# Kernel optimization log

Measured on AMD Instinct MI355X. Metric: run time of the kernel, lower is better.

## Reference

```python
import jax, jax.numpy as jnp
import numpy as np

DIM = 1024
NUM_HEADS = 16
HEAD_DIM = DIM // NUM_HEADS
SCALE = 1.0 / np.sqrt(HEAD_DIM)
B, S = 2, 2048


def setup_inputs() -> dict:
    key = jax.random.key(0)
    ks = jax.random.split(key, 10)
    std = 1.0 / np.sqrt(DIM)
    return {
        "x": jax.random.normal(ks[0], (B, S, DIM), dtype=jnp.float32),
        "Wq": jax.random.normal(ks[1], (DIM, DIM), dtype=jnp.float32) * std,
        "bq": jnp.zeros((DIM,), dtype=jnp.float32),
        "Wk": jax.random.normal(ks[2], (DIM, DIM), dtype=jnp.float32) * std,
        "bk": jnp.zeros((DIM,), dtype=jnp.float32),
        "Wv": jax.random.normal(ks[3], (DIM, DIM), dtype=jnp.float32) * std,
        "bv": jnp.zeros((DIM,), dtype=jnp.float32),
        "Wo": jax.random.normal(ks[4], (DIM, DIM), dtype=jnp.float32) * std,
        "bo": jnp.zeros((DIM,), dtype=jnp.float32),
        "mobius_weight": jax.random.normal(ks[5], (1,), dtype=jnp.float32) * 0.01,
    }


def _split_heads(t):
    b, s, _ = t.shape
    return t.reshape(b, s, NUM_HEADS, HEAD_DIM).transpose(0, 2, 1, 3)  # bhsd


def reference(x, Wq, bq, Wk, bk, Wv, bv, Wo, bo, mobius_weight):
    q = _split_heads(x @ Wq.T + bq)
    k = _split_heads(x @ Wk.T + bk)
    v = _split_heads(x @ Wv.T + bv)

    # similarity: plain QK^T
    similarity = jnp.einsum('bhqd,bhkd->bhqk', q, k)
    # mobius cross-term: q_omega . k_pi + q_pi . k_omega
    h = HEAD_DIM // 2
    q_om, q_pi = q[..., :h], q[..., h:]
    k_om, k_pi = k[..., :h], k[..., h:]
    mobius = jnp.einsum('bhqd,bhkd->bhqk', q_om, k_pi) + \
             jnp.einsum('bhqd,bhkd->bhqk', q_pi, k_om)

    incidence = (similarity + mobius_weight[0] * mobius) * SCALE
    attn = jax.nn.softmax(incidence, axis=-1)
    out = jnp.einsum('bhqk,bhkd->bhqd', attn, v)
    out = out.transpose(0, 2, 1, 3).reshape(x.shape[0], x.shape[1], DIM)
    return out @ Wo.T + bo
```

## Files before the change

### kernel.cpp

```cpp
#include <hip/hip_runtime.h>


typedef __attribute__((ext_vector_type(8))) short short8;
typedef __attribute__((ext_vector_type(4))) short s16x4;
typedef __attribute__((ext_vector_type(4))) float f32x4;
typedef __attribute__((ext_vector_type(16))) float f32x16;
typedef __attribute__((ext_vector_type(8))) __bf16 bf16x8;
typedef __attribute__((ext_vector_type(4))) unsigned uint4v;

__device__ __forceinline__ float exp2fa(float x) {
  return __builtin_amdgcn_exp2f(x);
}
__device__ __forceinline__ short f2bf(float f) {
  unsigned u = __builtin_bit_cast(unsigned, f);
  u = u + 0x7fffu + ((u >> 16) & 1u);
  return (short)(u >> 16);
}
__device__ __forceinline__ f32x4 mfma16(bf16x8 a, bf16x8 b, f32x4 c) {
  return __builtin_amdgcn_mfma_f32_16x16x32_bf16(a, b, c, 0, 0, 0);
}
__device__ __forceinline__ f32x16 mfma32(bf16x8 a, bf16x8 b, f32x16 c) {
  return __builtin_amdgcn_mfma_f32_32x32x16_bf16(a, b, c, 0, 0, 0);
}
__device__ __forceinline__ void gload_lds16(const void* g, void* l) {
  __builtin_amdgcn_global_load_lds(
      (const __attribute__((address_space(1))) unsigned int*)g,
      (__attribute__((address_space(3))) unsigned int*)l, 16, 0, 0);
}
__device__ __forceinline__ unsigned pkbf(float a, float b) {
  unsigned r;
  asm("v_cvt_pk_bf16_f32 %0, %1, %2" : "=v"(r) : "v"(a), "v"(b));
  return r;
}
__device__ __forceinline__ void plswap(unsigned& a, unsigned& b) {
  asm volatile("v_permlane32_swap_b32 %0, %1" : "+v"(a), "+v"(b));
}
__device__ __forceinline__ bf16x8 pack8(float x0, float x1, float x2, float x3,
                                        float x4, float x5, float x6, float x7) {
  unsigned a0 = pkbf(x0, x1), a1 = pkbf(x2, x3);
  unsigned a2 = pkbf(x4, x5), a3 = pkbf(x6, x7);
  plswap(a0, a2);
  plswap(a1, a3);
  uint4v u = {a0, a1, a2, a3};
  return __builtin_bit_cast(bf16x8, u);
}

__global__ void cast_all_kernel(const float* x, const float* w0, const float* w1,
                                const float* w2, const float* w3, short* xo,
                                short* o0, short* o1, short* o2, short* o3) {
  const float* in; short* out;
  const int r = blockIdx.y;
  size_t off;
  if (r < 4) { in = x; out = xo; off = (size_t)r * 131072; }
  else {
    switch (r) {
      case 4: in = w0; out = o0; break;
      case 5: in = w1; out = o1; break;
      case 6: in = w2; out = o2; break;
      default: in = w3; out = o3; break;
    }
    off = 0;
  }
  const size_t i = off + blockIdx.x * 256 + threadIdx.x;
  const float4* p = (const float4*)in;
  float4 a = p[2 * i], b = p[2 * i + 1];
  short8 o;
  o[0] = f2bf(a.x); o[1] = f2bf(a.y); o[2] = f2bf(a.z); o[3] = f2bf(a.w);
  o[4] = f2bf(b.x); o[5] = f2bf(b.y); o[6] = f2bf(b.z); o[7] = f2bf(b.w);
  ((short8*)out)[i] = o;
}

constexpr int GK = 1024, GN = 1024;
constexpr float QSCALE = 0.125f * 1.44269504088896340736f;

template <int EP>
__device__ __forceinline__ void gemm_body(char* lds, const short* __restrict__ A,
                                          const short* __restrict__ W,
                                          const float* __restrict__ bias,
                                          void* __restrict__ C,
                                          const float* __restrict__ mwp) {
  const int tid = threadIdx.x;
  const int l = tid & 63, w = tid >> 6;
  const int wr = w >> 1, wc = w & 1;
  const int m0 = blockIdx.y * 128, n0 = blockIdx.x * 128;

  f32x4 acc[4][4] = {};

  const int rg = l >> 3, c8 = l & 7;
  for (int kb = 0; kb < GK / 64; ++kb) {
    const int k0 = kb * 64;
#pragma unroll
    for (int i = 0; i < 4; ++i) {
      const int ra = i * 32 + w * 8 + rg;
      gload_lds16(A + (size_t)(m0 + ra) * GK + k0 + ((c8 ^ (ra & 7)) * 8),
                  lds + (i * 32 + w * 8) * 128);
      gload_lds16(W + (size_t)(n0 + ra) * GK + k0 + ((c8 ^ (ra & 7)) * 8),
                  lds + 16384 + (i * 32 + w * 8) * 128);
    }
    __syncthreads();
#pragma unroll
    for (int ks = 0; ks < 2; ++ks) {
      bf16x8 af[4], bfr[4];
      const int chunk = ks * 4 + (l >> 4);
#pragma unroll
      for (int mf = 0; mf < 4; ++mf) {
        const int mt = wr * 64 + mf * 16 + (l & 15);
        af[mf] = *(const bf16x8*)(lds + mt * 128 + ((chunk ^ (mt & 7)) * 16));
      }
#pragma unroll
      for (int nf = 0; nf < 4; ++nf) {
        const int nt = wc * 64 + nf * 16 + (l & 15);
        bfr[nf] = *(const bf16x8*)(lds + 16384 + nt * 128 + ((chunk ^ (nt & 7)) * 16));
      }
#pragma unroll
      for (int mf = 0; mf < 4; ++mf)
#pragma unroll
        for (int nf = 0; nf < 4; ++nf)
          acc[mf][nf] = mfma16(af[mf], bfr[nf], acc[mf][nf]);
    }
    __syncthreads();
  }

  const float mwv = (EP == 1) ? mwp[0] : 0.f;
#pragma unroll
  for (int mf = 0; mf < 4; ++mf)
#pragma unroll
    for (int nf = 0; nf < 4; ++nf) {
      const int n = n0 + wc * 64 + nf * 16 + (l & 15);
      const int mb = m0 + wr * 64 + mf * 16 + (l >> 4) * 4;
      if (EP == 2) {
        s16x4 v;
#pragma unroll
        for (int r = 0; r < 4; ++r) v[r] = f2bf(acc[mf][nf][r] + bias[n]);
        const int b = mb >> 11, s0 = mb & 2047;
        *(s16x4*)((short*)C + ((size_t)(b * 1024 + n)) * 2048 + s0) = v;
      } else {
        const float bv = bias[n];
#pragma unroll
        for (int r = 0; r < 4; ++r) {
          const int m = mb + r;
          float v = acc[mf][nf][r] + bv;
          if (EP == 0) v *= QSCALE;
          if (EP == 1) v += mwv * (acc[mf][nf ^ 2][r] + bias[n ^ 32]);
          if (EP == 3)
            ((float*)C)[(size_t)m * GN + n] = v;
          else
            ((short*)C)[(size_t)m * GN + n] = f2bf(v);
        }
      }
    }
}

__global__ __launch_bounds__(256) void gemm_qkv_kernel(
    const short* __restrict__ A, const short* Wq, const short* Wk, const short* Wv,
    const float* bq, const float* bk, const float* bv, short* q, short* kt,
    short* vt, const float* mw) {
  __shared__ __align__(16) char lds[32768];
  if (blockIdx.z == 0) gemm_body<0>(lds, A, Wq, bq, q, nullptr);
  else if (blockIdx.z == 1) gemm_body<1>(lds, A, Wk, bk, kt, mw);
  else gemm_body<2>(lds, A, Wv, bv, vt, nullptr);
}

__global__ __launch_bounds__(256) void gemm_out_kernel(const short* __restrict__ A,
                                                       const short* __restrict__ W,
                                                       const float* __restrict__ bias,
                                                       float* __restrict__ C) {
  __shared__ __align__(16) char lds[32768];
  gemm_body<3>(lds, A, W, bias, C, nullptr);
}

__global__ __launch_bounds__(512, 4) void attn_kernel(const short* __restrict__ Q,
                                                      const short* __restrict__ K,
                                                      const short* __restrict__ VT,
                                                      short* __restrict__ O) {
  constexpr int S = 2048;
  constexpr float FM = 16.0f;
  __shared__ __align__(16) char lds[4][16384];
  const int tid = threadIdx.x;
  const int l = tid & 63, w = tid >> 6;
  const int grp = w >> 2, w4 = w & 3;
  const int lo = l & 31, hi = l >> 5;
  const int bh = blockIdx.y, b = bh >> 4, h = bh & 15;
  const int q0 = blockIdx.x * 128 + w4 * 32;
  const size_t base = (size_t)b * S * 1024 + h * 64;
  const size_t vtrow0 = (size_t)(b * 1024 + h * 64);

  bf16x8 qf[4];
  {
    const short* qp = Q + base + (size_t)(q0 + lo) * 1024 + hi * 8;
#pragma unroll
    for (int ds = 0; ds < 4; ++ds) qf[ds] = *(const bf16x8*)(qp + ds * 16);
  }

  f32x16 o0 = {}, o1 = {};
  float lrow = 0.f;

  const int srow = tid >> 3, sc8 = tid & 7;
  auto STAGE = [&](int pr) {
#pragma unroll
    for (int g2 = 0; g2 < 2; ++g2) {
      const int t = 2 * pr + g2;
      char* Kd = lds[t & 3];
      char* Vd = lds[t & 3] + 8192;
      const int k0 = t * 64;
      gload_lds16(K + base + (size_t)(k0 + srow) * 1024 + ((sc8 ^ (srow & 7)) * 8),
                  Kd + w * 1024);
      gload_lds16(VT + (vtrow0 + srow) * 2048 + k0 + ((sc8 ^ (srow & 7)) * 8),
                  Vd + w * 1024);
    }
  };

  auto TILE = [&](const char* Kb, const char* Vb) {
    f32x16 st0, st1;
#pragma unroll
    for (int r = 0; r < 16; ++r) { st0[r] = -FM; st1[r] = -FM; }
    __builtin_amdgcn_s_setprio(1);
#pragma unroll
    for (int ds = 0; ds < 4; ++ds) {
      const int c = ds * 2 + hi;
      bf16x8 kf0 = *(const bf16x8*)(Kb + lo * 128 + ((c ^ (lo & 7)) * 16));
      bf16x8 kf1 = *(const bf16x8*)(Kb + (32 + lo) * 128 + ((c ^ (lo & 7)) * 16));
      st0 = mfma32(kf0, qf[ds], st0);
      st1 = mfma32(kf1, qf[ds], st1);
    }
    __builtin_amdgcn_s_setprio(0);

#pragma unroll
    for (int r = 0; r < 16; ++r) st0[r] = exp2fa(st0[r]);
#pragma unroll
    for (int r = 0; r < 16; ++r) st1[r] = exp2fa(st1[r]);
    float ts[8];
#pragma unroll
    for (int r = 0; r < 8; ++r)
      ts[r] = (st0[r] + st0[r + 8]) + (st1[r] + st1[r + 8]);
#pragma unroll
    for (int d = 4; d >= 1; d >>= 1)
#pragma unroll
      for (int r = 0; r < 4; ++r)
        if (r < d) ts[r] += ts[r + d];
    lrow += ts[0] + __shfl_xor(ts[0], 32);

    bf16x8 pf[4];
    pf[0] = pack8(st0[0], st0[1], st0[2], st0[3], st0[4], st0[5], st0[6], st0[7]);
    pf[1] = pack8(st0[8], st0[9], st0[10], st0[11], st0[12], st0[13], st0[14], st0[15]);
    pf[2] = pack8(st1[0], st1[1], st1[2], st1[3], st1[4], st1[5], st1[6], st1[7]);
    pf[3] = pack8(st1[8], st1[9], st1[10], st1[11], st1[12], st1[13], st1[14], st1[15]);

    __builtin_amdgcn_s_setprio(1);
#pragma unroll
    for (int kv = 0; kv < 4; ++kv) {
      const int c = kv * 2 + hi;
      bf16x8 vf0 = *(const bf16x8*)(Vb + lo * 128 + ((c ^ (lo & 7)) * 16));
      bf16x8 vf1 = *(const bf16x8*)(Vb + (32 + lo) * 128 + ((c ^ (lo & 7)) * 16));
      o0 = mfma32(vf0, pf[kv], o0);
      o1 = mfma32(vf1, pf[kv], o1);
    }
    __builtin_amdgcn_s_setprio(0);
  };

  STAGE(0);
  for (int p = 0; p < S / 128; ++p) {
    if (p < S / 128 - 1) {
      STAGE(p + 1);
      asm volatile("s_waitcnt vmcnt(4)" ::: "memory");
    } else {
      asm volatile("s_waitcnt vmcnt(0)" ::: "memory");
    }
    __builtin_amdgcn_s_barrier();
    const char* buf = lds[(2 * p + grp) & 3];
    TILE(buf, buf + 8192);
    asm volatile("" ::: "memory");
    __builtin_amdgcn_s_barrier();
  }

  __syncthreads();
  float* mbuf = (float*)&lds[0][0];
  float* lbuf = (float*)&lds[2][0];
  if (grp == 1) {
#pragma unroll
    for (int g = 0; g < 4; ++g) {
      const int c0 = (2 * g + hi) ^ (lo & 15);
      const int c1 = (8 + 2 * g + hi) ^ (lo & 15);
      f32x4 v0, v1;
#pragma unroll
      for (int r = 0; r < 4; ++r) { v0[r] = o0[g * 4 + r]; v1[r] = o1[g * 4 + r]; }
      *(f32x4*)(mbuf + (w4 * 32 + lo) * 64 + c0 * 4) = v0;
      *(f32x4*)(mbuf + (w4 * 32 + lo) * 64 + c1 * 4) = v1;
    }
    if (hi == 0) lbuf[w4 * 32 + lo] = lrow;
  }
  __syncthreads();
  if (grp == 0) {
#pragma unroll
    for (int g = 0; g < 4; ++g) {
      const int c0 = (2 * g + hi) ^ (lo & 15);
      const int c1 = (8 + 2 * g + hi) ^ (lo & 15);
      f32x4 v0 = *(const f32x4*)(mbuf + (w4 * 32 + lo) * 64 + c0 * 4);
      f32x4 v1 = *(const f32x4*)(mbuf + (w4 * 32 + lo) * 64 + c1 * 4);
#pragma unroll
      for (int r = 0; r < 4; ++r) { o0[g * 4 + r] += v0[r]; o1[g * 4 + r] += v1[r]; }
    }
    const float inv = 1.0f / (lrow + lbuf[w4 * 32 + lo]);
    short* Op = O + base + (size_t)(q0 + lo) * 1024;
#pragma unroll
    for (int g = 0; g < 4; ++g) {
      s16x4 v0, v1;
#pragma unroll
      for (int r = 0; r < 4; ++r) {
        v0[r] = f2bf(o0[g * 4 + r] * inv);
        v1[r] = f2bf(o1[g * 4 + r] * inv);
      }
      *(s16x4*)(Op + 8 * g + 4 * hi) = v0;
      *(s16x4*)(Op + 32 + 8 * g + 4 * hi) = v1;
    }
  }
}

extern "C" void kernel_launch(void* const* d_in, const int* in_sizes, int n_in,
                              void* d_out, int out_size, void* d_ws, size_t ws_size,
                              hipStream_t stream) {
  const float* x  = (const float*)d_in[0];
  const float* Wq = (const float*)d_in[1];
  const float* bq = (const float*)d_in[2];
  const float* Wk = (const float*)d_in[3];
  const float* bk = (const float*)d_in[4];
  const float* Wv = (const float*)d_in[5];
  const float* bv = (const float*)d_in[6];
  const float* Wo = (const float*)d_in[7];
  const float* bo = (const float*)d_in[8];
  const float* mw = (const float*)d_in[9];
  float* out = (float*)d_out;
  char* ws = (char*)d_ws;
  const size_t MB = (size_t)1 << 20;

  short* xb  = (short*)(ws + 0 * MB);
  short* wqb = (short*)(ws + 8 * MB);
  short* wkb = (short*)(ws + 10 * MB);
  short* wvb = (short*)(ws + 12 * MB);
  short* wob = (short*)(ws + 14 * MB);
  short* qb  = (short*)(ws + 16 * MB);
  short* ktb = (short*)(ws + 24 * MB);
  short* vtb = (short*)(ws + 32 * MB);
  short* ob  = (short*)(ws + 40 * MB);

  cast_all_kernel<<<dim3(512, 8), 256, 0, stream>>>(x, Wq, Wk, Wv, Wo, xb, wqb,
                                                    wkb, wvb, wob);
  gemm_qkv_kernel<<<dim3(8, 32, 3), 256, 0, stream>>>(xb, wqb, wkb, wvb, bq, bk, bv,
                                                      qb, ktb, vtb, mw);
  attn_kernel<<<dim3(16, 32), 512, 0, stream>>>(qb, ktb, vtb, ob);
  gemm_out_kernel<<<dim3(8, 32), 256, 0, stream>>>(ob, wob, bo, out);
}
```

Baseline: 131.9 us.

## Store K/V in MFMA-fragment order and load directly to registers, dropping LDS staging

The QKV GEMM epilogue now writes K and V in a pre-swizzled, fragment-ordered layout per head, so each attention lane can read its MFMA operands with contiguous 16-byte global loads. The attention kernel drops the LDS staging, barriers and waitcnt pipeline, instead prefetching the next K/V tile into registers during compute. Blocks shrink to 256 threads covering 64 queries, with a remapped 1D grid for L2 locality across heads. The kernel also removes the -16 softmax offset by initialising scores to zero. This trades LDS reuse across waves for more redundant global/L2 traffic and higher register pressure.

```diff
diff --git a/kernel.cpp b/kernel.cpp
--- a/kernel.cpp
+++ b/kernel.cpp
@@ -128,12 +128,26 @@
     for (int nf = 0; nf < 4; ++nf) {
       const int n = n0 + wc * 64 + nf * 16 + (l & 15);
       const int mb = m0 + wr * 64 + mf * 16 + (l >> 4) * 4;
-      if (EP == 2) {
+      if (EP == 1) {
+        const float bv = bias[n], bv2 = bias[n ^ 32];
+        const int h = n >> 6, c = (n >> 3) & 7, j = n & 7;
+#pragma unroll
+        for (int r = 0; r < 4; ++r) {
+          const int m = mb + r;
+          const int b = m >> 11, s = m & 2047;
+          const float v =
+              acc[mf][nf][r] + bv + mwv * (acc[mf][nf ^ 2][r] + bv2);
+          ((short*)C)[(size_t)(b * 16 + h) * 131072 + (s >> 5) * 2048 + c * 256 +
+                      (s & 31) * 8 + j] = f2bf(v);
+        }
+      } else if (EP == 2) {
+        const int h = n >> 6, w2 = (n >> 5) & 1, dlo = n & 31;
         s16x4 v;
 #pragma unroll
         for (int r = 0; r < 4; ++r) v[r] = f2bf(acc[mf][nf][r] + bias[n]);
-        const int b = mb >> 11, s0 = mb & 2047;
-        *(s16x4*)((short*)C + ((size_t)(b * 1024 + n)) * 2048 + s0) = v;
+        const int b = mb >> 11, s = mb & 2047;
+        *(s16x4*)((short*)C + (size_t)(b * 16 + h) * 131072 + (s >> 6) * 4096 +
+                  w2 * 2048 + ((s >> 3) & 7) * 256 + dlo * 8 + (s & 7)) = v;
       } else {
         const float bv = bias[n];
 #pragma unroll
@@ -141,7 +155,6 @@
           const int m = mb + r;
           float v = acc[mf][nf][r] + bv;
           if (EP == 0) v *= QSCALE;
-          if (EP == 1) v += mwv * (acc[mf][nf ^ 2][r] + bias[n ^ 32]);
           if (EP == 3)
             ((float*)C)[(size_t)m * GN + n] = v;
           else
@@ -153,12 +166,12 @@
 
 __global__ __launch_bounds__(256) void gemm_qkv_kernel(
     const short* __restrict__ A, const short* Wq, const short* Wk, const short* Wv,
-    const float* bq, const float* bk, const float* bv, short* q, short* kt,
-    short* vt, const float* mw) {
+    const float* bq, const float* bk, const float* bv, short* q, short* kf,
+    short* vf, const float* mw) {
   __shared__ __align__(16) char lds[32768];
   if (blockIdx.z == 0) gemm_body<0>(lds, A, Wq, bq, q, nullptr);
-  else if (blockIdx.z == 1) gemm_body<1>(lds, A, Wk, bk, kt, mw);
-  else gemm_body<2>(lds, A, Wv, bv, vt, nullptr);
+  else if (blockIdx.z == 1) gemm_body<1>(lds, A, Wk, bk, kf, mw);
+  else gemm_body<2>(lds, A, Wv, bv, vf, nullptr);
 }
 
 __global__ __launch_bounds__(256) void gemm_out_kernel(const short* __restrict__ A,
@@ -169,21 +182,25 @@
   gemm_body<3>(lds, A, W, bias, C, nullptr);
 }
 
-__global__ __launch_bounds__(512, 4) void attn_kernel(const short* __restrict__ Q,
-                                                      const short* __restrict__ K,
-                                                      const short* __restrict__ VT,
+__global__ __launch_bounds__(256, 3) void attn_kernel(const short* __restrict__ Q,
+                                                      const short* __restrict__ Kf,
+                                                      const short* __restrict__ Vf,
                                                       short* __restrict__ O) {
   constexpr int S = 2048;
-  constexpr float FM = 16.0f;
-  __shared__ __align__(16) char lds[4][16384];
+  __shared__ float mbuf[2][32][64];
+  __shared__ float lbuf[64];
   const int tid = threadIdx.x;
   const int l = tid & 63, w = tid >> 6;
-  const int grp = w >> 2, w4 = w & 3;
   const int lo = l & 31, hi = l >> 5;
-  const int bh = blockIdx.y, b = bh >> 4, h = bh & 15;
-  const int q0 = blockIdx.x * 128 + w4 * 32;
+  const int wq = w & 1, par = w >> 1;
+  const int bid = blockIdx.x;
+  const int sub = bid >> 3;
+  const int x = sub & 31;
+  const int y = (bid & 7) * 4 + (sub >> 5);
+  const int b = y >> 4, h = y & 15;
+  const int q0 = x * 64 + wq * 32;
   const size_t base = (size_t)b * S * 1024 + h * 64;
-  const size_t vtrow0 = (size_t)(b * 1024 + h * 64);
+  const size_t fbase = (size_t)y * 131072;
 
   bf16x8 qf[4];
   {
@@ -192,38 +209,39 @@
     for (int ds = 0; ds < 4; ++ds) qf[ds] = *(const bf16x8*)(qp + ds * 16);
   }
 
+  const int voff = hi * 256 + lo * 8;
+  const short* kp = Kf + fbase + par * 4096 + voff;
+  const short* vp = Vf + fbase + par * 4096 + voff;
+
+  bf16x8 kf[8], vf[8];
+#pragma unroll
+  for (int ds = 0; ds < 4; ++ds) {
+    kf[ds]     = *(const bf16x8*)(kp + ds * 512);
+    kf[4 + ds] = *(const bf16x8*)(kp + 2048 + ds * 512);
+    vf[ds]     = *(const bf16x8*)(vp + ds * 512);
+    vf[4 + ds] = *(const bf16x8*)(vp + 2048 + ds * 512);
+  }
+
   f32x16 o0 = {}, o1 = {};
   float lrow = 0.f;
 
-  const int srow = tid >> 3, sc8 = tid & 7;
-  auto STAGE = [&](int pr) {
-#pragma unroll
-    for (int g2 = 0; g2 < 2; ++g2) {
-      const int t = 2 * pr + g2;
-      char* Kd = lds[t & 3];
-      char* Vd = lds[t & 3] + 8192;
-      const int k0 = t * 64;
-      gload_lds16(K + base + (size_t)(k0 + srow) * 1024 + ((sc8 ^ (srow & 7)) * 8),
-                  Kd + w * 1024);
-      gload_lds16(VT + (vtrow0 + srow) * 2048 + k0 + ((sc8 ^ (srow & 7)) * 8),
-                  Vd + w * 1024);
-    }
-  };
-
-  auto TILE = [&](const char* Kb, const char* Vb) {
-    f32x16 st0, st1;
-#pragma unroll
-    for (int r = 0; r < 16; ++r) { st0[r] = -FM; st1[r] = -FM; }
+  for (int i = 0; i < S / 128; ++i) {
+    f32x16 st0 = {}, st1 = {};
     __builtin_amdgcn_s_setprio(1);
 #pragma unroll
     for (int ds = 0; ds < 4; ++ds) {
-      const int c = ds * 2 + hi;
-      bf16x8 kf0 = *(const bf16x8*)(Kb + lo * 128 + ((c ^ (lo & 7)) * 16));
-      bf16x8 kf1 = *(const bf16x8*)(Kb + (32 + lo) * 128 + ((c ^ (lo & 7)) * 16));
-      st0 = mfma32(kf0, qf[ds], st0);
-      st1 = mfma32(kf1, qf[ds], st1);
+      st0 = mfma32(kf[ds], qf[ds], st0);
+      st1 = mfma32(kf[4 + ds], qf[ds], st1);
     }
     __builtin_amdgcn_s_setprio(0);
+    if (i + 1 < S / 128) {
+      kp += 8192;
+#pragma unroll
+      for (int ds = 0; ds < 4; ++ds) {
+        kf[ds]     = *(const bf16x8*)(kp + ds * 512);
+        kf[4 + ds] = *(const bf16x8*)(kp + 2048 + ds * 512);
+      }
+    }
 
 #pragma unroll
     for (int r = 0; r < 16; ++r) st0[r] = exp2fa(st0[r]);
@@ -249,34 +267,21 @@
     __builtin_amdgcn_s_setprio(1);
 #pragma unroll
     for (int kv = 0; kv < 4; ++kv) {
-      const int c = kv * 2 + hi;
-      bf16x8 vf0 = *(const bf16x8*)(Vb + lo * 128 + ((c ^ (lo & 7)) * 16));
-      bf16x8 vf1 = *(const bf16x8*)(Vb + (32 + lo) * 128 + ((c ^ (lo & 7)) * 16));
-      o0 = mfma32(vf0, pf[kv], o0);
-      o1 = mfma32(vf1, pf[kv], o1);
+      o0 = mfma32(vf[kv], pf[kv], o0);
+      o1 = mfma32(vf[4 + kv], pf[kv], o1);
     }
     __builtin_amdgcn_s_setprio(0);
-  };
-
-  STAGE(0);
-  for (int p = 0; p < S / 128; ++p) {
-    if (p < S / 128 - 1) {
-      STAGE(p + 1);
-      asm volatile("s_waitcnt vmcnt(4)" ::: "memory");
-    } else {
-      asm volatile("s_waitcnt vmcnt(0)" ::: "memory");
-    }
-    __builtin_amdgcn_s_barrier();
-    const char* buf = lds[(2 * p + grp) & 3];
-    TILE(buf, buf + 8192);
-    asm volatile("" ::: "memory");
-    __builtin_amdgcn_s_barrier();
-  }
-
-  __syncthreads();
-  float* mbuf = (float*)&lds[0][0];
-  float* lbuf = (float*)&lds[2][0];
-  if (grp == 1) {
+    if (i + 1 < S / 128) {
+      vp += 8192;
+#pragma unroll
+      for (int kv = 0; kv < 4; ++kv) {
+        vf[kv]     = *(const bf16x8*)(vp + kv * 512);
+        vf[4 + kv] = *(const bf16x8*)(vp + 2048 + kv * 512);
+      }
+    }
+  }
+
+  if (par == 1) {
 #pragma unroll
     for (int g = 0; g < 4; ++g) {
       const int c0 = (2 * g + hi) ^ (lo & 15);
@@ -284,23 +289,23 @@
       f32x4 v0, v1;
 #pragma unroll
       for (int r = 0; r < 4; ++r) { v0[r] = o0[g * 4 + r]; v1[r] = o1[g * 4 + r]; }
-      *(f32x4*)(mbuf + (w4 * 32 + lo) * 64 + c0 * 4) = v0;
-      *(f32x4*)(mbuf + (w4 * 32 + lo) * 64 + c1 * 4) = v1;
-    }
-    if (hi == 0) lbuf[w4 * 32 + lo] = lrow;
+      *(f32x4*)(&mbuf[wq][lo][c0 * 4]) = v0;
+      *(f32x4*)(&mbuf[wq][lo][c1 * 4]) = v1;
+    }
+    if (hi == 0) lbuf[wq * 32 + lo] = lrow;
   }
   __syncthreads();
-  if (grp == 0) {
+  if (par == 0) {
 #pragma unroll
     for (int g = 0; g < 4; ++g) {
       const int c0 = (2 * g + hi) ^ (lo & 15);
       const int c1 = (8 + 2 * g + hi) ^ (lo & 15);
-      f32x4 v0 = *(const f32x4*)(mbuf + (w4 * 32 + lo) * 64 + c0 * 4);
-      f32x4 v1 = *(const f32x4*)(mbuf + (w4 * 32 + lo) * 64 + c1 * 4);
+      f32x4 v0 = *(const f32x4*)(&mbuf[wq][lo][c0 * 4]);
+      f32x4 v1 = *(const f32x4*)(&mbuf[wq][lo][c1 * 4]);
 #pragma unroll
       for (int r = 0; r < 4; ++r) { o0[g * 4 + r] += v0[r]; o1[g * 4 + r] += v1[r]; }
     }
-    const float inv = 1.0f / (lrow + lbuf[w4 * 32 + lo]);
+    const float inv = 1.0f / (lrow + lbuf[wq * 32 + lo]);
     short* Op = O + base + (size_t)(q0 + lo) * 1024;
 #pragma unroll
     for (int g = 0; g < 4; ++g) {
@@ -339,14 +344,14 @@
   short* wvb = (short*)(ws + 12 * MB);
   short* wob = (short*)(ws + 14 * MB);
   short* qb  = (short*)(ws + 16 * MB);
-  short* ktb = (short*)(ws + 24 * MB);
-  short* vtb = (short*)(ws + 32 * MB);
+  short* kfb = (short*)(ws + 24 * MB);
+  short* vfb = (short*)(ws + 32 * MB);
   short* ob  = (short*)(ws + 40 * MB);
 
   cast_all_kernel<<<dim3(512, 8), 256, 0, stream>>>(x, Wq, Wk, Wv, Wo, xb, wqb,
                                                     wkb, wvb, wob);
   gemm_qkv_kernel<<<dim3(8, 32, 3), 256, 0, stream>>>(xb, wqb, wkb, wvb, bq, bk, bv,
-                                                      qb, ktb, vtb, mw);
-  attn_kernel<<<dim3(16, 32), 512, 0, stream>>>(qb, ktb, vtb, ob);
+                                                      qb, kfb, vfb, mw);
+  attn_kernel<<<1024, 256, 0, stream>>>(qb, kfb, vfb, ob);
   gemm_out_kernel<<<dim3(8, 32), 256, 0, stream>>>(ob, wob, bo, out);
 }
```

Result: faster. 126.0 us (-4.5%).
